# Kernel optimization log

Measured on AMD Instinct MI355X. Metric: run time of the kernel, lower is better.

The kernel has to match this reference:

```python
import jax, jax.numpy as jnp
import numpy as np

N = 50000          # nodes
E = 1_600_000      # edges (avg degree 32)
F_IN = 256
F_OUT = 256
ALPHA = 0.2        # LeakyReLU negative slope


def setup_inputs() -> dict:
    key = jax.random.key(0)
    ks = jax.random.split(key, 7)
    x = jax.random.normal(ks[0], (N, F_IN), dtype=jnp.float32)
    row = jax.random.randint(ks[1], (E,), 0, N, dtype=jnp.int32)  # dst i
    col = jax.random.randint(ks[2], (E,), 0, N, dtype=jnp.int32)  # src j
    W_w = jax.random.normal(ks[3], (F_IN, F_OUT), dtype=jnp.float32) / np.sqrt(F_IN).astype(np.float32)
    W_b = jax.random.normal(ks[4], (F_OUT,), dtype=jnp.float32) * 0.01
    a_w = jax.random.normal(ks[5], (2 * F_OUT,), dtype=jnp.float32) / np.sqrt(2 * F_OUT).astype(np.float32)
    a_b = jax.random.normal(ks[6], (1,), dtype=jnp.float32) * 0.01
    return {"x": x, "W_w": W_w, "W_b": W_b, "a_w": a_w, "a_b": a_b,
            "row": row, "col": col}


def reference(x, W_w, W_b, a_w, a_b, row, col):
    # Wh = W(x): [N, F_OUT]
    Wh = x @ W_w + W_b
    # e[i,j] = leakyrelu(a1 . Wh[j] + a2 . Wh[i] + b)
    # (repeat puts Wh[j] in the first half of the concat, repeat_interleave Wh[i] in the second)
    f_dst_part = Wh @ a_w[:F_OUT]   # contribution of column node j
    f_row_part = Wh @ a_w[F_OUT:]   # contribution of row node i
    e = f_dst_part[col] + f_row_part[row] + a_b[0]          # [E]
    e = jnp.where(e > 0, e, ALPHA * e)                      # LeakyReLU
    # sparse softmax over dim=1 (segment = row i), adjacency values are 1.0
    m = jax.ops.segment_max(e, row, num_segments=N)         # [N]
    ex = jnp.exp(e - m[row])
    denom = jax.ops.segment_sum(ex, row, num_segments=N)    # [N]
    att = ex / denom[row]                                   # [E]
    # h'[i] = sum_j att[i,j] * Wh[j]  (spmm), empty rows stay zero
    h_prime = jax.ops.segment_sum(att[:, None] * Wh[col], row, num_segments=N)
    return jax.nn.relu(h_prime)
```

## Files before the change

kernel.cpp:

```cpp
#include <hip/hip_runtime.h>
#include <math.h>

#define N_NODES 50000
#define N_EDGES 1600000
#define F 256
#define ALPHA 0.2f
#define NP 50048
#define NB 196
#define CAP 10240
#define EPB 4096
#define NAB ((N_EDGES + EPB - 1) / EPB)
#define GEMM_BLOCKS 782
#define FVEC_SLOTS 2048
#define PULL_BLOCKS 2048

typedef short bf16x8 __attribute__((ext_vector_type(8)));
typedef float f32x4 __attribute__((ext_vector_type(4)));
typedef _Float16 half4 __attribute__((ext_vector_type(4)));
typedef _Float16 half8 __attribute__((ext_vector_type(8)));

__device__ __forceinline__ unsigned short f2bf(float f) {
  union { float f; unsigned u; } v; v.f = f;
  unsigned u = v.u;
  return (unsigned short)((u + 0x7fffu + ((u >> 16) & 1u)) >> 16);
}

__device__ __forceinline__ unsigned short f2h_bits(float f) {
  union { _Float16 h; unsigned short u; } v;
  v.h = (_Float16)f;
  return v.u;
}

__device__ __forceinline__ float h_bits2f(unsigned short u) {
  union { _Float16 h; unsigned short u; } v;
  v.u = u;
  return (float)v.h;
}

__global__ __launch_bounds__(256) void prep_w(const float* __restrict__ W,
                                              const float* __restrict__ a_w,
                                              const float* __restrict__ W_b,
                                              const float* __restrict__ a_b,
                                              unsigned short* __restrict__ Wt,
                                              float* __restrict__ wa,
                                              float* __restrict__ cb,
                                              int* __restrict__ gcur) {
  if (blockIdx.x == 64) {
    if (threadIdx.x < NB) gcur[threadIdx.x] = 0;
    return;
  }
  const int lane = threadIdx.x & 63, w = threadIdx.x >> 6;
  const int k = blockIdx.x * 4 + w;
  float4 wv = *(const float4*)(W + (size_t)k * F + lane * 4);
  float4 a1 = *(const float4*)(a_w + lane * 4);
  float4 a2 = *(const float4*)(a_w + F + lane * 4);
  Wt[(size_t)(lane * 4 + 0) * F + k] = f2bf(wv.x);
  Wt[(size_t)(lane * 4 + 1) * F + k] = f2bf(wv.y);
  Wt[(size_t)(lane * 4 + 2) * F + k] = f2bf(wv.z);
  Wt[(size_t)(lane * 4 + 3) * F + k] = f2bf(wv.w);
  float s1 = wv.x * a1.x + wv.y * a1.y + wv.z * a1.z + wv.w * a1.w;
  float s2 = wv.x * a2.x + wv.y * a2.y + wv.z * a2.z + wv.w * a2.w;
#pragma unroll
  for (int off = 32; off > 0; off >>= 1) {
    s1 += __shfl_down(s1, off, 64);
    s2 += __shfl_down(s2, off, 64);
  }
  if (lane == 0) { wa[k] = s1; wa[F + k] = s2; }
  if (blockIdx.x == 0 && w == 0) {
    float4 b = *(const float4*)(W_b + lane * 4);
    float t1 = b.x * (a1.x + a2.x) + b.y * (a1.y + a2.y) +
               b.z * (a1.z + a2.z) + b.w * (a1.w + a2.w);
#pragma unroll
    for (int off = 32; off > 0; off >>= 1) t1 += __shfl_down(t1, off, 64);
    if (lane == 0) cb[0] = t1 + a_b[0];
  }
}

#define LDSK 72
__global__ __launch_bounds__(256) void gemm_fvec_binA2(
    const float* __restrict__ x,
    const unsigned short* __restrict__ Wt,
    const float* __restrict__ bias,
    const float* __restrict__ wa,
    const int* __restrict__ row,
    const int* __restrict__ col,
    _Float16* __restrict__ Wh,
    float* __restrict__ f_dst,
    float* __restrict__ f_row,
    int* __restrict__ gcur,
    unsigned* __restrict__ gstage) {
  __shared__ char smem[2 * 128 * LDSK * 2];
  if (blockIdx.x < GEMM_BLOCKS) {
    short* As = (short*)smem;
    short* Bs = As + 128 * LDSK;
    const int tid = threadIdx.x;
    const int lane = tid & 63;
    const int w = tid >> 6;
    const int wm = w >> 1, wn = w & 1;
    const int m0 = (blockIdx.x >> 1) * 128;
    const int n0 = (blockIdx.x & 1) * 128;
    f32x4 acc[4][4] = {{{0.f, 0.f, 0.f, 0.f}}};
    const int srow = tid >> 3;
    const int schunk = tid & 7;
    for (int k0 = 0; k0 < F; k0 += 64) {
#pragma unroll
      for (int i = 0; i < 4; ++i) {
        int r = i * 32 + srow;
        int gm = m0 + r; if (gm > N_NODES - 1) gm = N_NODES - 1;
        const float* src = x + (size_t)gm * F + k0 + schunk * 8;
        float4 lo = *(const float4*)src;
        float4 hi = *(const float4*)(src + 4);
        bf16x8 v;
        v[0] = (short)f2bf(lo.x); v[1] = (short)f2bf(lo.y);
        v[2] = (short)f2bf(lo.z); v[3] = (short)f2bf(lo.w);
        v[4] = (short)f2bf(hi.x); v[5] = (short)f2bf(hi.y);
        v[6] = (short)f2bf(hi.z); v[7] = (short)f2bf(hi.w);
        *(bf16x8*)&As[r * LDSK + schunk * 8] = v;
        *(bf16x8*)&Bs[r * LDSK + schunk * 8] =
            *(const bf16x8*)(Wt + (size_t)(n0 + r) * F + k0 + schunk * 8);
      }
      __syncthreads();
#pragma unroll
      for (int kk = 0; kk < 64; kk += 32) {
        const int rowsel = lane & 15;
        const int ksel = kk + (lane >> 4) * 8;
        bf16x8 af[4], bfr[4];
#pragma unroll
        for (int t = 0; t < 4; ++t) {
          af[t] = *(bf16x8*)&As[(wm * 64 + t * 16 + rowsel) * LDSK + ksel];
          bfr[t] = *(bf16x8*)&Bs[(wn * 64 + t * 16 + rowsel) * LDSK + ksel];
        }
#pragma unroll
        for (int mi = 0; mi < 4; ++mi)
#pragma unroll
          for (int nj = 0; nj < 4; ++nj)
            acc[mi][nj] = __builtin_amdgcn_mfma_f32_16x16x32_bf16(
                af[mi], bfr[nj], acc[mi][nj], 0, 0, 0);
      }
      __syncthreads();
    }
    const int crow = (lane >> 4) * 4;
    const int ccol = lane & 15;
#pragma unroll
    for (int nj = 0; nj < 4; ++nj) {
      int gc = n0 + wn * 64 + nj * 16 + ccol;
      float bv = bias[gc];
#pragma unroll
      for (int mi = 0; mi < 4; ++mi) {
        int gr = m0 + wm * 64 + mi * 16 + crow;
#pragma unroll
        for (int r = 0; r < 4; ++r)
          Wh[(size_t)(gr + r) * F + gc] = (_Float16)(acc[mi][nj][r] + bv);
      }
    }
    return;
  }
  if (blockIdx.x < GEMM_BLOCKS + NAB) {
    int* h = (int*)smem;
    int* lofs = h + NB;
    int* lcur = lofs + NB;
    int* gb = lcur + NB;
    unsigned* stage = (unsigned*)(gb + NB);
    const int t = threadIdx.x;
    for (int i = t; i < NB; i += 256) { h[i] = 0; lcur[i] = 0; }
    __syncthreads();
    const int base = (blockIdx.x - GEMM_BLOCKS) * EPB;
    const int cnt = min(EPB, N_EDGES - base);
#pragma unroll
    for (int j = 0; j < 16; ++j) {
      int k = base + j * 256 + t;
      if (k < N_EDGES) atomicAdd(&h[row[k] >> 8], 1);
    }
    __syncthreads();
    if (t == 0) {
      int run = 0;
      for (int i = 0; i < NB; ++i) { lofs[i] = run; run += h[i]; }
    }
    __syncthreads();
    if (t < NB && h[t] > 0) gb[t] = atomicAdd(&gcur[t], h[t]);
    __syncthreads();
#pragma unroll
    for (int j = 0; j < 16; ++j) {
      int k = base + j * 256 + t;
      if (k < N_EDGES) {
        int r = row[k], b = r >> 8;
        int lp = lofs[b] + atomicAdd(&lcur[b], 1);
        stage[lp] = ((unsigned)b << 24) | ((unsigned)(r & 255) << 16) |
                    (unsigned)col[k];
      }
    }
    __syncthreads();
#pragma unroll
    for (int j = 0; j < 16; ++j) {
      int s = j * 256 + t;
      if (s < cnt) {
        unsigned wv = stage[s];
        int b = wv >> 24;
        gstage[(size_t)b * CAP + gb[b] + (s - lofs[b])] = wv & 0x00FFFFFFu;
      }
    }
    return;
  }
  const int lane = threadIdx.x & 63, w = threadIdx.x >> 6;
  const int slot = blockIdx.x - GEMM_BLOCKS - NAB;
  float4 v1 = *(const float4*)(wa + lane * 4);
  float4 v2 = *(const float4*)(wa + F + lane * 4);
  for (int node = slot * 4 + w; node < N_NODES; node += FVEC_SLOTS * 4) {
    float4 xv = *(const float4*)(x + (size_t)node * F + lane * 4);
    float s1 = xv.x * v1.x + xv.y * v1.y + xv.z * v1.z + xv.w * v1.w;
    float s2 = xv.x * v2.x + xv.y * v2.y + xv.z * v2.z + xv.w * v2.w;
#pragma unroll
    for (int off = 32; off > 0; off >>= 1) {
      s1 += __shfl_down(s1, off, 64);
      s2 += __shfl_down(s2, off, 64);
    }
    if (lane == 0) { f_dst[node] = s1; f_row[node] = s2; }
  }
}

__global__ __launch_bounds__(512) void binB(const int* __restrict__ gcur,
                                            const unsigned* __restrict__ gstage,
                                            const float* __restrict__ f_dst,
                                            const float* __restrict__ f_row,
                                            const float* __restrict__ cb,
                                            int2* __restrict__ rsc,
                                            float* __restrict__ inv_denom,
                                            unsigned* __restrict__ csr) {
  __shared__ int cnt2[2048];
  __shared__ int cur2[2048];
  __shared__ int rcnt[256], rbase[256];
  __shared__ float dsum[256];
  const int t = threadIdx.x;
  const int b = blockIdx.x;
  for (int i = t; i < 2048; i += 512) cnt2[i] = 0;
  if (t < 256) dsum[t] = 0.f;
  __syncthreads();
  const int nb = gcur[b];
  const int start = b * CAP;
  const float cbs = cb[0];
  for (int s = t; s < nb; s += 512) {
    unsigned wv = gstage[start + s];
    int key = (((wv >> 16) & 255) << 3) | ((wv & 0xFFFFu) >> 13);
    atomicAdd(&cnt2[key], 1);
  }
  __syncthreads();
  if (t < 256) {
    int tot = 0;
#pragma unroll
    for (int q = 0; q < 8; ++q) tot += cnt2[t * 8 + q];
    rcnt[t] = tot;
  }
  __syncthreads();
  if (t == 0) {
    int run = 0;
    for (int i = 0; i < 256; ++i) { rbase[i] = run; run += rcnt[i]; }
  }
  __syncthreads();
  if (t < 256) {
    int base = start + rbase[t];
    int g = (b << 8) + t;
    if (g < N_NODES) rsc[g] = make_int2(base, rcnt[t]);
    int run = base;
#pragma unroll
    for (int q = 0; q < 8; ++q) { cur2[t * 8 + q] = run; run += cnt2[t * 8 + q]; }
  }
  __syncthreads();
  for (int s = t; s < nb; s += 512) {
    unsigned wv = gstage[start + s];
    int lr = (wv >> 16) & 255;
    int c = wv & 0xFFFF;
    float ev = f_dst[c] + f_row[(b << 8) + lr] + cbs;
    ev = ev > 0.f ? ev : ALPHA * ev;
    float ex = __expf(ev);
    int p = atomicAdd(&cur2[(lr << 3) | (c >> 13)], 1);
    csr[p] = ((unsigned)f2h_bits(ex) << 16) | (unsigned)c;
    atomicAdd(&dsum[lr], ex);
  }
  __syncthreads();
  if (t < 256) {
    int g = (b << 8) + t;
    if (g < N_NODES) inv_denom[g] = (rcnt[t] > 0) ? (1.0f / dsum[t]) : 0.f;
  }
}

__global__ __launch_bounds__(256) void gat_pull(const int2* __restrict__ rsc,
                                                const unsigned* __restrict__ csr,
                                                const float* __restrict__ inv_denom,
                                                const _Float16* __restrict__ Wh,
                                                float* __restrict__ out) {
  const int lane = threadIdx.x & 63;
  const int eo = lane >> 5;
  const int l32 = lane & 31;
  const int wid = blockIdx.x * 4 + (threadIdx.x >> 6);
  const int nw = PULL_BLOCKS * 4;
  const char* whb = (const char*)Wh;
  const unsigned chanoff = (unsigned)l32 * 16u;
  for (int i = wid; i < N_NODES; i += nw) {
    const int2 rc = rsc[i];
    const int s = rc.x, e = rc.x + rc.y;
    float acc[8] = {0.f, 0.f, 0.f, 0.f, 0.f, 0.f, 0.f, 0.f};
    int p = s;
    for (; p + 16 <= e; p += 16) {
      unsigned wv[8];
#pragma unroll
      for (int j = 0; j < 8; ++j) wv[j] = csr[p + 2 * j + eo];
      half8 v[8];
#pragma unroll
      for (int j = 0; j < 8; ++j) {
        unsigned off = (wv[j] & 0xFFFFu) * 512u + chanoff;
        v[j] = *(const half8*)(whb + off);
      }
#pragma unroll
      for (int j = 0; j < 8; ++j) {
        float xw = h_bits2f((unsigned short)(wv[j] >> 16));
#pragma unroll
        for (int c = 0; c < 8; ++c) acc[c] += xw * (float)v[j][c];
      }
    }
    for (; p < e; p += 4) {
      int q0 = p + eo, q1 = p + 2 + eo;
      unsigned w0 = csr[q0 < e ? q0 : s];
      unsigned w1 = csr[q1 < e ? q1 : s];
      unsigned off0 = (w0 & 0xFFFFu) * 512u + chanoff;
      unsigned off1 = (w1 & 0xFFFFu) * 512u + chanoff;
      half8 v0 = *(const half8*)(whb + off0);
      half8 v1 = *(const half8*)(whb + off1);
      float xw0 = (q0 < e) ? h_bits2f((unsigned short)(w0 >> 16)) : 0.f;
      float xw1 = (q1 < e) ? h_bits2f((unsigned short)(w1 >> 16)) : 0.f;
#pragma unroll
      for (int c = 0; c < 8; ++c) acc[c] += xw0 * (float)v0[c];
#pragma unroll
      for (int c = 0; c < 8; ++c) acc[c] += xw1 * (float)v1[c];
    }
#pragma unroll
    for (int c = 0; c < 8; ++c) acc[c] += __shfl_xor(acc[c], 32, 64);
    const float inv = inv_denom[i];
    float r0 = eo ? acc[4] : acc[0];
    float r1 = eo ? acc[5] : acc[1];
    float r2 = eo ? acc[6] : acc[2];
    float r3 = eo ? acc[7] : acc[3];
    float4 o = make_float4(fmaxf(r0 * inv, 0.f), fmaxf(r1 * inv, 0.f),
                           fmaxf(r2 * inv, 0.f), fmaxf(r3 * inv, 0.f));
    ((float4*)out)[(size_t)i * 64 + l32 * 2 + eo] = o;
  }
}

extern "C" void kernel_launch(void* const* d_in, const int* in_sizes, int n_in,
                              void* d_out, int out_size, void* d_ws, size_t ws_size,
                              hipStream_t stream) {
  const float* x   = (const float*)d_in[0];
  const float* W_w = (const float*)d_in[1];
  const float* W_b = (const float*)d_in[2];
  const float* a_w = (const float*)d_in[3];
  const float* a_b = (const float*)d_in[4];
  const int*   row = (const int*)d_in[5];
  const int*   col = (const int*)d_in[6];
  float* out = (float*)d_out;

  float* ws = (float*)d_ws;
  size_t off = 0;
  _Float16* Wh = (_Float16*)(ws + off); off += (size_t)NP * F / 2;
  unsigned short* Wt = (unsigned short*)(ws + off); off += (F * F) / 2;
  float* wa = ws + off;            off += 2 * F;
  float* cb = ws + off;            off += 8;
  float* f_dst = ws + off;         off += NP;
  float* f_row = ws + off;         off += NP;
  int* gcur = (int*)(ws + off);    off += NB;
  int2* rsc = (int2*)(ws + off);   off += 2 * (size_t)NP;
  float* inv_denom = (float*)(ws + off); off += NP;
  unsigned* gstage = (unsigned*)(ws + off); off += (size_t)NB * CAP;
  unsigned* csr = (unsigned*)(ws + off); off += (size_t)NB * CAP;
  (void)ws_size; (void)in_sizes; (void)n_in; (void)out_size;

  hipLaunchKernelGGL(prep_w, dim3(65), dim3(256), 0, stream, W_w, a_w, W_b,
                     a_b, Wt, wa, cb, gcur);
  hipLaunchKernelGGL(gemm_fvec_binA2, dim3(GEMM_BLOCKS + NAB + FVEC_SLOTS),
                     dim3(256), 0, stream, x, Wt, W_b, wa, row, col, Wh,
                     f_dst, f_row, gcur, gstage);
  hipLaunchKernelGGL(binB, dim3(NB), dim3(512), 0, stream, gcur, gstage,
                     f_dst, f_row, cb, rsc, inv_denom, csr);
  hipLaunchKernelGGL(gat_pull, dim3(PULL_BLOCKS), dim3(256), 0, stream,
                     rsc, csr, inv_denom, Wh, out);
}
```

Measured before the change: 285.0 us.

## Interleave pull over column bins across multiple rows per wave for Wh locality

binB now records the start offset of each of a row's eight column-range sub-bins. gat_pull has each wave own up to seven rows and walk them bin by bin, so all waves gather Wh rows from the same column range at roughly the same time. The goal is better L2 and MALL hit rates on the random Wh gathers. The cost is more registers for seven accumulator sets, extra bstart traffic, shorter inner loops with more tail handling, and possibly lower occupancy.

```diff
diff --git a/kernel.cpp b/kernel.cpp
--- a/kernel.cpp
+++ b/kernel.cpp
@@ -13,6 +13,9 @@
 #define GEMM_BLOCKS 782
 #define FVEC_SLOTS 2048
 #define PULL_BLOCKS 2048
+#define NW_TOT (PULL_BLOCKS * 4)
+#define NPW 7
+#define NBIN 8
 
 typedef short bf16x8 __attribute__((ext_vector_type(8)));
 typedef float f32x4 __attribute__((ext_vector_type(4)));
@@ -225,7 +228,8 @@
                                             const float* __restrict__ cb,
                                             int2* __restrict__ rsc,
                                             float* __restrict__ inv_denom,
-                                            unsigned* __restrict__ csr) {
+                                            unsigned* __restrict__ csr,
+                                            int* __restrict__ bstart) {
   __shared__ int cnt2[2048];
   __shared__ int cur2[2048];
   __shared__ int rcnt[256], rbase[256];
@@ -261,8 +265,17 @@
     int g = (b << 8) + t;
     if (g < N_NODES) rsc[g] = make_int2(base, rcnt[t]);
     int run = base;
-#pragma unroll
-    for (int q = 0; q < 8; ++q) { cur2[t * 8 + q] = run; run += cnt2[t * 8 + q]; }
+    int bs[8];
+#pragma unroll
+    for (int q = 0; q < 8; ++q) {
+      cur2[t * 8 + q] = run;
+      bs[q] = run;
+      run += cnt2[t * 8 + q];
+    }
+    if (g < N_NODES) {
+      *(int4*)&bstart[(size_t)g * 8]     = make_int4(bs[0], bs[1], bs[2], bs[3]);
+      *(int4*)&bstart[(size_t)g * 8 + 4] = make_int4(bs[4], bs[5], bs[6], bs[7]);
+    }
   }
   __syncthreads();
   for (int s = t; s < nb; s += 512) {
@@ -286,59 +299,85 @@
 __global__ __launch_bounds__(256) void gat_pull(const int2* __restrict__ rsc,
                                                 const unsigned* __restrict__ csr,
                                                 const float* __restrict__ inv_denom,
+                                                const int* __restrict__ bstart,
                                                 const _Float16* __restrict__ Wh,
                                                 float* __restrict__ out) {
   const int lane = threadIdx.x & 63;
   const int eo = lane >> 5;
   const int l32 = lane & 31;
   const int wid = blockIdx.x * 4 + (threadIdx.x >> 6);
-  const int nw = PULL_BLOCKS * 4;
   const char* whb = (const char*)Wh;
   const unsigned chanoff = (unsigned)l32 * 16u;
-  for (int i = wid; i < N_NODES; i += nw) {
-    const int2 rc = rsc[i];
-    const int s = rc.x, e = rc.x + rc.y;
-    float acc[8] = {0.f, 0.f, 0.f, 0.f, 0.f, 0.f, 0.f, 0.f};
-    int p = s;
-    for (; p + 16 <= e; p += 16) {
-      unsigned wv[8];
-#pragma unroll
-      for (int j = 0; j < 8; ++j) wv[j] = csr[p + 2 * j + eo];
-      half8 v[8];
-#pragma unroll
-      for (int j = 0; j < 8; ++j) {
-        unsigned off = (wv[j] & 0xFFFFu) * 512u + chanoff;
-        v[j] = *(const half8*)(whb + off);
-      }
-#pragma unroll
-      for (int j = 0; j < 8; ++j) {
-        float xw = h_bits2f((unsigned short)(wv[j] >> 16));
-#pragma unroll
-        for (int c = 0; c < 8; ++c) acc[c] += xw * (float)v[j][c];
-      }
-    }
-    for (; p < e; p += 4) {
-      int q0 = p + eo, q1 = p + 2 + eo;
-      unsigned w0 = csr[q0 < e ? q0 : s];
-      unsigned w1 = csr[q1 < e ? q1 : s];
-      unsigned off0 = (w0 & 0xFFFFu) * 512u + chanoff;
-      unsigned off1 = (w1 & 0xFFFFu) * 512u + chanoff;
-      half8 v0 = *(const half8*)(whb + off0);
-      half8 v1 = *(const half8*)(whb + off1);
-      float xw0 = (q0 < e) ? h_bits2f((unsigned short)(w0 >> 16)) : 0.f;
-      float xw1 = (q1 < e) ? h_bits2f((unsigned short)(w1 >> 16)) : 0.f;
-#pragma unroll
-      for (int c = 0; c < 8; ++c) acc[c] += xw0 * (float)v0[c];
-#pragma unroll
-      for (int c = 0; c < 8; ++c) acc[c] += xw1 * (float)v1[c];
-    }
-#pragma unroll
-    for (int c = 0; c < 8; ++c) acc[c] += __shfl_xor(acc[c], 32, 64);
+  float acc[NPW][8];
+  int p[NPW], pend[NPW];
+#pragma unroll
+  for (int jn = 0; jn < NPW; ++jn) {
+#pragma unroll
+    for (int c = 0; c < 8; ++c) acc[jn][c] = 0.f;
+    int i = wid + jn * NW_TOT;
+    if (i < N_NODES) {
+      int2 rc = rsc[i];
+      p[jn] = rc.x;
+      pend[jn] = rc.x + rc.y;
+    } else {
+      p[jn] = 0; pend[jn] = 0;
+    }
+  }
+  for (int q = 0; q < NBIN; ++q) {
+#pragma unroll
+    for (int jn = 0; jn < NPW; ++jn) {
+      int i = wid + jn * NW_TOT;
+      if (i >= N_NODES) continue;
+      int pe = (q < NBIN - 1) ? bstart[(size_t)i * 8 + q + 1] : pend[jn];
+      int pp = p[jn];
+      if (pp >= pe) { p[jn] = pe; continue; }
+      const int s0 = pp;
+      for (; pp + 8 <= pe; pp += 8) {
+        unsigned wv[4];
+#pragma unroll
+        for (int j = 0; j < 4; ++j) wv[j] = csr[pp + 2 * j + eo];
+        half8 v[4];
+#pragma unroll
+        for (int j = 0; j < 4; ++j) {
+          unsigned off = (wv[j] & 0xFFFFu) * 512u + chanoff;
+          v[j] = *(const half8*)(whb + off);
+        }
+#pragma unroll
+        for (int j = 0; j < 4; ++j) {
+          float xw = h_bits2f((unsigned short)(wv[j] >> 16));
+#pragma unroll
+          for (int c = 0; c < 8; ++c) acc[jn][c] += xw * (float)v[j][c];
+        }
+      }
+      for (; pp < pe; pp += 4) {
+        int q0 = pp + eo, q1 = pp + 2 + eo;
+        unsigned w0 = csr[q0 < pe ? q0 : s0];
+        unsigned w1 = csr[q1 < pe ? q1 : s0];
+        unsigned off0 = (w0 & 0xFFFFu) * 512u + chanoff;
+        unsigned off1 = (w1 & 0xFFFFu) * 512u + chanoff;
+        half8 v0 = *(const half8*)(whb + off0);
+        half8 v1 = *(const half8*)(whb + off1);
+        float xw0 = (q0 < pe) ? h_bits2f((unsigned short)(w0 >> 16)) : 0.f;
+        float xw1 = (q1 < pe) ? h_bits2f((unsigned short)(w1 >> 16)) : 0.f;
+#pragma unroll
+        for (int c = 0; c < 8; ++c) acc[jn][c] += xw0 * (float)v0[c];
+#pragma unroll
+        for (int c = 0; c < 8; ++c) acc[jn][c] += xw1 * (float)v1[c];
+      }
+      p[jn] = pe;
+    }
+  }
+#pragma unroll
+  for (int jn = 0; jn < NPW; ++jn) {
+    int i = wid + jn * NW_TOT;
+    if (i >= N_NODES) continue;
+#pragma unroll
+    for (int c = 0; c < 8; ++c) acc[jn][c] += __shfl_xor(acc[jn][c], 32, 64);
     const float inv = inv_denom[i];
-    float r0 = eo ? acc[4] : acc[0];
-    float r1 = eo ? acc[5] : acc[1];
-    float r2 = eo ? acc[6] : acc[2];
-    float r3 = eo ? acc[7] : acc[3];
+    float r0 = eo ? acc[jn][4] : acc[jn][0];
+    float r1 = eo ? acc[jn][5] : acc[jn][1];
+    float r2 = eo ? acc[jn][6] : acc[jn][2];
+    float r3 = eo ? acc[jn][7] : acc[jn][3];
     float4 o = make_float4(fmaxf(r0 * inv, 0.f), fmaxf(r1 * inv, 0.f),
                            fmaxf(r2 * inv, 0.f), fmaxf(r3 * inv, 0.f));
     ((float4*)out)[(size_t)i * 64 + l32 * 2 + eo] = o;
@@ -370,6 +409,7 @@
   float* inv_denom = (float*)(ws + off); off += NP;
   unsigned* gstage = (unsigned*)(ws + off); off += (size_t)NB * CAP;
   unsigned* csr = (unsigned*)(ws + off); off += (size_t)NB * CAP;
+  int* bstart = (int*)(ws + off);  off += (size_t)NP * 8;
   (void)ws_size; (void)in_sizes; (void)n_in; (void)out_size;
 
   hipLaunchKernelGGL(prep_w, dim3(65), dim3(256), 0, stream, W_w, a_w, W_b,
@@ -378,7 +418,7 @@
                      dim3(256), 0, stream, x, Wt, W_b, wa, row, col, Wh,
                      f_dst, f_row, gcur, gstage);
   hipLaunchKernelGGL(binB, dim3(NB), dim3(512), 0, stream, gcur, gstage,
-                     f_dst, f_row, cb, rsc, inv_denom, csr);
+                     f_dst, f_row, cb, rsc, inv_denom, csr, bstart);
   hipLaunchKernelGGL(gat_pull, dim3(PULL_BLOCKS), dim3(256), 0, stream,
-                     rsc, csr, inv_denom, Wh, out);
-}
+                     rsc, csr, inv_denom, bstart, Wh, out);
+}
```

After: 492.2 us. 1.73x slower.
